# Performance work log

Hardware: AMD Instinct MI355X
Metric: run time of the kernel (lower is better)

The kernel has to match this reference:

```python
import jax, jax.numpy as jnp
import numpy as np

B, S, D = 2, 2048, 1024          # batch, seq, n_embd
E, GS, K = 8, 4, 2               # num_experts, group_size, top-k
H = 2 * D                        # hidden_dim of SharedExpertMLP
A = H // 16                      # adapt_dim = 128
G = E // GS                      # num_groups
LN_EPS = 1e-5


def _ln(z, g, b):
    mu = jnp.mean(z, -1, keepdims=True)
    v = jnp.mean((z - mu) ** 2, -1, keepdims=True)
    return (z - mu) * jax.lax.rsqrt(v + LN_EPS) * g + b


def setup_inputs() -> dict:
    key = jax.random.key(0)
    ks = jax.random.split(key, 12)
    s = float(D) ** -0.5
    sa = s * 0.01
    se = 0.01 * float(A) ** -0.5
    n = lambda k, shape, std: jax.random.normal(k, shape, jnp.float32) * std
    return {
        'x': jax.random.normal(ks[0], (B, S, D), jnp.float32),
        'W_up': n(ks[1], (H, D), s),
        'W_gate': n(ks[2], (H, D), s),
        'W_down': n(ks[3], (D, H), s),
        'W_pre': n(ks[4], (A, D), sa),
        'W_post': n(ks[5], (A, H), sa),
        'ln_g': jnp.ones((A,), jnp.float32),
        'ln_b': jnp.zeros((A,), jnp.float32),
        'W_aproj': n(ks[6], (H, A), sa),
        'A_exp': n(ks[7], (E, A, A), se),
        'ln_g_e': jnp.ones((E, A), jnp.float32),
        'ln_b_e': jnp.zeros((E, A), jnp.float32),
        'W_eproj': n(ks[8], (H, A), se),
        'W_oproj': n(ks[9], (D, H), se),
        'W_rg': n(ks[10], (G, D), 0.001),
        'W_re': n(ks[11], (GS, D), 0.001),
    }


def reference(x, W_up, W_gate, W_down, W_pre, W_post, ln_g, ln_b, W_aproj,
              A_exp, ln_g_e, ln_b_e, W_eproj, W_oproj, W_rg, W_re):
    silu = jax.nn.silu
    # ---- SharedExpertMLP ----
    up = x @ W_up.T
    gate = x @ W_gate.T
    hidden = silu(gate) * up                               # [B,S,H]
    adapt_in = _ln(x @ W_pre.T, ln_g, ln_b)                # [B,S,A]
    adapt_out = _ln(hidden @ W_post.T, ln_g, ln_b)         # [B,S,A]
    aw = silu(jnp.clip(jnp.einsum('bsa,bta->bst', adapt_in, adapt_out), -5.0, 5.0))
    adapt = jnp.einsum('bst,bta->bsa', aw, adapt_in)
    hidden = hidden + 0.1 * (adapt @ W_aproj.T)
    shared = hidden @ W_down.T                             # [B,S,D]
    # ---- HierarchicalRouter ----
    gl = x @ W_rg.T                                        # [B,S,G]
    gp = jax.nn.softmax(gl, -1)
    gw = jnp.max(gp, -1)                                   # top-1 group weight
    gidx = jnp.argmax(gp, -1)
    el = x @ W_re.T                                        # [B,S,GS]
    ep = jax.nn.softmax(el, -1)
    wloc, iloc = jax.lax.top_k(ep, K)
    eidx = gidx[..., None] * GS + iloc                     # [B,S,K] global expert ids
    wloc = wloc / (jnp.sum(wloc, -1, keepdims=True) + 1e-7)
    fw = gw[..., None] * wloc                              # final weights
    N = B * S
    dm = jnp.zeros((N, E), x.dtype).at[
        jnp.arange(N)[:, None], eidx.reshape(N, K)].set(fw.reshape(N, K))
    load = dm.sum(0)
    target = load.sum() / E
    router_loss = 0.001 * (jnp.mean((load - target) ** 2)
                           + jnp.mean(gl ** 2) + jnp.mean(el ** 2))
    dm = dm.reshape(B, S, E)
    # ---- ExpertGroup combine (vectorized masked gather/MLP/scatter) ----
    pre = x @ W_pre.T                                      # [B,S,A]
    h_e = jnp.einsum('bsa,eca->ebsc', pre, A_exp)          # per-expert adapter
    h_e = _ln(h_e, ln_g_e[:, None, None, :], ln_b_e[:, None, None, :])
    contrib = jnp.einsum('ebsc,hc->ebsh', h_e, W_eproj)    # [E,B,S,H]
    contrib = jnp.einsum('ebsh,dh->ebsd', contrib, W_oproj)
    w_e = jnp.moveaxis(dm, -1, 0)                          # [E,B,S]
    out = jnp.sum(dm, -1)[..., None] * shared + 0.1 * jnp.einsum('ebsd,ebs->bsd', contrib, w_e)
    return out, router_loss
```

## Files before the change

kernel.cpp:

```cpp
#include <hip/hip_runtime.h>
#include <hip/hip_bf16.h>
#include <math.h>

static constexpr int Bc = 2;
static constexpr int Sc = 2048;
static constexpr int Dc = 1024;
static constexpr int Hc = 2048;
static constexpr int Ac = 128;
static constexpr int Ec = 8;
static constexpr int GSc = 4;
static constexpr int Gc = 2;
static constexpr int Nc = Bc * Sc;
static constexpr float LN_EPSc = 1e-5f;
static constexpr int RBLK = 512;

typedef __attribute__((ext_vector_type(8))) short bf16x8;
typedef __attribute__((ext_vector_type(4))) float f32x4;
typedef __attribute__((ext_vector_type(4))) unsigned short us4;

__device__ __forceinline__ unsigned short f2b(float f) {
    union { float f; unsigned u; } v; v.f = f;
    return (unsigned short)((v.u + 0x7FFFu + ((v.u >> 16) & 1u)) >> 16);
}
__device__ __forceinline__ float b2f(unsigned short h) {
    union { unsigned u; float f; } v; v.u = (unsigned)h << 16; return v.f;
}
__device__ __forceinline__ float fsilu(float x) {
    return x / (1.f + __expf(-x));
}

#define GLOAD16(g, l) __builtin_amdgcn_global_load_lds( \
    (const __attribute__((address_space(1))) void*)(g), \
    (__attribute__((address_space(3))) void*)(l), 16, 0, 0)

template<int EPI>
__global__ __launch_bounds__(256, 4) void mgemm(
    const unsigned short* __restrict__ Ag, const unsigned short* __restrict__ Bg,
    void* __restrict__ Cg, int N, int K, int lda, int ldb, float alpha,
    float* __restrict__ aux, void* __restrict__ aux2,
    long long sA, long long sB, long long sC)
{
    __shared__ unsigned short As[128 * 64];
    __shared__ unsigned short Bs[128 * 64];
    const unsigned short* A = Ag + (long long)blockIdx.z * sA;
    const unsigned short* B = Bg + (long long)blockIdx.z * sB;
    float* fC = (float*)Cg + (long long)blockIdx.z * sC;
    unsigned short* usC = (unsigned short*)Cg + (long long)blockIdx.z * sC;

    const int nwg = gridDim.x * gridDim.y;
    const int flat = blockIdx.y * gridDim.x + blockIdx.x;
    const int swz = (flat & 7) * (nwg >> 3) + (flat >> 3);
    const int bx = swz % gridDim.x, by = swz / gridDim.x;
    const int bm = by * 128, bn = bx * 128;

    const int tid = threadIdx.x;
    const int w = tid >> 6, l = tid & 63;
    const int wm = (w >> 1) * 64, wn = (w & 1) * 64;
    const int fr = l & 15, g = l >> 4;

    const f32x4 zero = { 0.f, 0.f, 0.f, 0.f };
    f32x4 acc[4][4];
    #pragma unroll
    for (int i = 0; i < 4; ++i)
        #pragma unroll
        for (int j = 0; j < 4; ++j) acc[i][j] = zero;

    for (int k0 = 0; k0 < K; k0 += 64) {
        #pragma unroll
        for (int p = 0; p < 4; ++p) {
            const int c = p * 256 + tid;
            const int row = c >> 3;
            const int gch = (c & 7) ^ ((c >> 4) & 7);
            GLOAD16(A + (long long)(bm + row) * lda + k0 + gch * 8, &As[c * 8]);
            GLOAD16(B + (long long)(bn + row) * ldb + k0 + gch * 8, &Bs[c * 8]);
        }
        __syncthreads();
        #pragma unroll
        for (int h = 0; h < 2; ++h) {
            bf16x8 af[4], bfv[4];
            #pragma unroll
            for (int i = 0; i < 4; ++i) {
                const int ra = wm + i * 16 + fr;
                af[i]  = *(const bf16x8*)&As[ra * 64 + ((h * 4 + g) ^ ((ra >> 1) & 7)) * 8];
                const int rb = wn + i * 16 + fr;
                bfv[i] = *(const bf16x8*)&Bs[rb * 64 + ((h * 4 + g) ^ ((rb >> 1) & 7)) * 8];
            }
            #pragma unroll
            for (int i = 0; i < 4; ++i)
                #pragma unroll
                for (int j = 0; j < 4; ++j)
                    acc[i][j] = __builtin_amdgcn_mfma_f32_16x16x32_bf16(af[i], bfv[j], acc[i][j], 0, 0, 0);
        }
        __syncthreads();
    }

    if (EPI == 9) {
        if (bn < 2 * Hc) {
            #pragma unroll
            for (int mi = 0; mi < 4; ++mi) {
                #pragma unroll
                for (int j = 0; j < 2; ++j) {
                    #pragma unroll
                    for (int jr = 0; jr < 4; ++jr) {
                        const long long row = bm + wm + mi * 16 + g * 4 + jr;
                        const long long colh = ((bn + wn) >> 1) + j * 16 + fr;
                        const float gv = acc[mi][2 * j][jr];
                        const float uv = acc[mi][2 * j + 1][jr];
                        usC[row * Hc + colh] = f2b(fsilu(gv) * uv);
                    }
                }
            }
        } else {
            unsigned short* preb = (unsigned short*)aux2;
            #pragma unroll
            for (int mi = 0; mi < 4; ++mi) {
                #pragma unroll
                for (int ni = 0; ni < 4; ++ni) {
                    #pragma unroll
                    for (int jr = 0; jr < 4; ++jr) {
                        const long long row = bm + wm + mi * 16 + g * 4 + jr;
                        const int lc = wn + ni * 16 + fr;
                        const float v = acc[mi][ni][jr];
                        aux[row * Ac + lc] = v;
                        preb[row * Ac + lc] = f2b(v);
                    }
                }
            }
        }
    } else {
        #pragma unroll
        for (int mi = 0; mi < 4; ++mi)
            #pragma unroll
            for (int ni = 0; ni < 4; ++ni)
                #pragma unroll
                for (int jr = 0; jr < 4; ++jr) {
                    const long long row = bm + wm + mi * 16 + g * 4 + jr;
                    const long long col = bn + wn + ni * 16 + fr;
                    const long long idx = row * (long long)N + col;
                    const float v = acc[mi][ni][jr];
                    if (EPI == 0) fC[idx] = v;
                    else usC[idx] = f2b(alpha * v);
                }
    }
}

__global__ __launch_bounds__(256, 2) void mgemm64(
    const unsigned short* __restrict__ Ag, const unsigned short* __restrict__ Bg,
    float* __restrict__ Cg, int N, int K, int lda, int ldb, int zmod,
    long long sA1, long long sB1, long long sC1,
    long long sA2, long long sB2, long long sC2)
{
    __shared__ unsigned short As[128 * 32];
    __shared__ unsigned short Bs[64 * 32];
    const int z1 = blockIdx.z % zmod, z2 = blockIdx.z / zmod;
    const unsigned short* A = Ag + (long long)z1 * sA1 + (long long)z2 * sA2;
    const unsigned short* B = Bg + (long long)z1 * sB1 + (long long)z2 * sB2;
    float* fC = Cg + (long long)z1 * sC1 + (long long)z2 * sC2;

    const int nwg = gridDim.x * gridDim.y;
    const int flat = blockIdx.y * gridDim.x + blockIdx.x;
    const int swz = (flat & 7) * (nwg >> 3) + (flat >> 3);
    const int bx = swz % gridDim.x, by = swz / gridDim.x;
    const int bm = by * 128, bn = bx * 64;

    const int tid = threadIdx.x;
    const int w = tid >> 6, l = tid & 63;
    const int wm = (w >> 1) * 64, wn = (w & 1) * 32;
    const int fr = l & 15, g = l >> 4;

    const f32x4 zero = { 0.f, 0.f, 0.f, 0.f };
    f32x4 acc[4][2];
    #pragma unroll
    for (int i = 0; i < 4; ++i)
        #pragma unroll
        for (int j = 0; j < 2; ++j) acc[i][j] = zero;

    for (int k0 = 0; k0 < K; k0 += 32) {
        #pragma unroll
        for (int p = 0; p < 2; ++p) {
            const int c = p * 256 + tid;
            GLOAD16(A + (long long)(bm + (c >> 2)) * lda + k0 + (c & 3) * 8, &As[c * 8]);
        }
        GLOAD16(B + (long long)(bn + (tid >> 2)) * ldb + k0 + (tid & 3) * 8, &Bs[tid * 8]);
        __syncthreads();
        bf16x8 af[4], bfv[2];
        #pragma unroll
        for (int i = 0; i < 4; ++i)
            af[i]  = *(const bf16x8*)&As[(wm + i * 16 + fr) * 32 + g * 8];
        #pragma unroll
        for (int j = 0; j < 2; ++j)
            bfv[j] = *(const bf16x8*)&Bs[(wn + j * 16 + fr) * 32 + g * 8];
        #pragma unroll
        for (int i = 0; i < 4; ++i)
            #pragma unroll
            for (int j = 0; j < 2; ++j)
                acc[i][j] = __builtin_amdgcn_mfma_f32_16x16x32_bf16(af[i], bfv[j], acc[i][j], 0, 0, 0);
        __syncthreads();
    }

    #pragma unroll
    for (int mi = 0; mi < 4; ++mi)
        #pragma unroll
        for (int ni = 0; ni < 2; ++ni)
            #pragma unroll
            for (int jr = 0; jr < 4; ++jr) {
                const long long row = bm + wm + mi * 16 + g * 4 + jr;
                const long long col = bn + wn + ni * 16 + fr;
                fC[row * (long long)N + col] = acc[mi][ni][jr];
            }
}

__global__ __launch_bounds__(256, 2) void fadapt_k(
    const unsigned short* __restrict__ adapt_in,
    const unsigned short* __restrict__ adapt_out,
    const unsigned short* __restrict__ adapt_inT,
    float* __restrict__ partial)
{
    __shared__ unsigned short P_lds[4 * 64 * 32];

    const int b = blockIdx.z;
    const int q0 = blockIdx.y * 64;
    const int t0 = blockIdx.x * 256;

    const unsigned short* Qg = adapt_in + (long long)b * Sc * Ac;
    const unsigned short* Kg = adapt_out + (long long)b * Sc * Ac;
    const unsigned short* Vt = adapt_inT + (long long)b * Ac * Sc;

    const int tid = threadIdx.x;
    const int w = tid >> 6, l = tid & 63;
    const int wm = (w >> 1) * 32, wn = (w & 1) * 64;
    const int fr = l & 15, g = l >> 4;

    bf16x8 qf[2][4];
    #pragma unroll
    for (int i = 0; i < 2; ++i) {
        const long long ra = q0 + wm + i * 16 + fr;
        #pragma unroll
        for (int ks = 0; ks < 4; ++ks)
            qf[i][ks] = *(const bf16x8*)&Qg[ra * Ac + ks * 32 + g * 8];
    }

    const f32x4 zero = { 0.f, 0.f, 0.f, 0.f };
    f32x4 acc[2][4];
    #pragma unroll
    for (int i = 0; i < 2; ++i)
        #pragma unroll
        for (int j = 0; j < 4; ++j) acc[i][j] = zero;

    #pragma unroll 1
    for (int ts = 0; ts < 2; ++ts) {
        const int t1 = t0 + ts * 128;
        f32x4 sacc[2][4];
        #pragma unroll
        for (int i = 0; i < 2; ++i)
            #pragma unroll
            for (int j = 0; j < 4; ++j) sacc[i][j] = zero;
        #pragma unroll
        for (int ks = 0; ks < 4; ++ks) {
            bf16x8 bfv[4];
            #pragma unroll
            for (int j = 0; j < 4; ++j) {
                const long long rb = t1 + wn + j * 16 + fr;
                bfv[j] = *(const bf16x8*)&Kg[rb * Ac + ks * 32 + g * 8];
            }
            #pragma unroll
            for (int i = 0; i < 2; ++i)
                #pragma unroll
                for (int j = 0; j < 4; ++j)
                    sacc[i][j] = __builtin_amdgcn_mfma_f32_16x16x32_bf16(qf[i][ks], bfv[j], sacc[i][j], 0, 0, 0);
        }
        __syncthreads();
        #pragma unroll
        for (int mi = 0; mi < 2; ++mi) {
            #pragma unroll
            for (int ni = 0; ni < 4; ++ni) {
                const int t = wn + ni * 16 + fr;
                const int tl = t & 31;
                const int kbase = (t >> 5) * 2048;
                #pragma unroll
                for (int jr = 0; jr < 4; ++jr) {
                    const int row = wm + mi * 16 + g * 4 + jr;
                    float v = sacc[mi][ni][jr];
                    v = fminf(fmaxf(v, -5.f), 5.f);
                    const int pos = (((tl >> 3) ^ ((row >> 1) & 3)) << 3) + (tl & 7);
                    P_lds[kbase + row * 32 + pos] = f2b(fsilu(v));
                }
            }
        }
        __syncthreads();
        #pragma unroll
        for (int ks = 0; ks < 4; ++ks) {
            bf16x8 af[2], bfv[4];
            #pragma unroll
            for (int i = 0; i < 2; ++i) {
                const int ra = wm + i * 16 + fr;
                af[i] = *(const bf16x8*)&P_lds[ks * 2048 + ra * 32 + (g ^ ((ra >> 1) & 3)) * 8];
            }
            #pragma unroll
            for (int j = 0; j < 4; ++j) {
                const long long rb = wn + j * 16 + fr;
                bfv[j] = *(const bf16x8*)&Vt[rb * Sc + t1 + ks * 32 + g * 8];
            }
            #pragma unroll
            for (int i = 0; i < 2; ++i)
                #pragma unroll
                for (int j = 0; j < 4; ++j)
                    acc[i][j] = __builtin_amdgcn_mfma_f32_16x16x32_bf16(af[i], bfv[j], acc[i][j], 0, 0, 0);
        }
    }

    float* op = partial + ((long long)blockIdx.x * Bc + b) * Sc * Ac;
    #pragma unroll
    for (int mi = 0; mi < 2; ++mi)
        #pragma unroll
        for (int ni = 0; ni < 4; ++ni)
            #pragma unroll
            for (int jr = 0; jr < 4; ++jr) {
                const long long row = q0 + wm + mi * 16 + g * 4 + jr;
                const long long col = wn + ni * 16 + fr;
                op[row * Ac + col] = acc[mi][ni][jr];
            }
}

__global__ __launch_bounds__(256, 2) void final_k(
    const unsigned short* __restrict__ hidden, const unsigned short* __restrict__ Wd,
    const unsigned short* __restrict__ adaptb, const unsigned short* __restrict__ Wdap,
    const unsigned short* __restrict__ h2v, const unsigned short* __restrict__ Wopep,
    const float* __restrict__ dmsum, float* __restrict__ out)
{
    __shared__ unsigned short As[128 * 64];
    __shared__ unsigned short Bs[64 * 64];

    const int nwg = gridDim.x * gridDim.y;
    const int flat = blockIdx.y * gridDim.x + blockIdx.x;
    const int swz = (flat & 7) * (nwg >> 3) + (flat >> 3);
    const int bx = swz % gridDim.x, by = swz / gridDim.x;
    const int bm = by * 128, bn = bx * 64;

    const int tid = threadIdx.x;
    const int w = tid >> 6, l = tid & 63;
    const int wm = (w >> 1) * 64, wn = (w & 1) * 32;
    const int fr = l & 15, g = l >> 4;

    const f32x4 zero = { 0.f, 0.f, 0.f, 0.f };
    f32x4 acc[4][2];
    #pragma unroll
    for (int i = 0; i < 4; ++i)
        #pragma unroll
        for (int j = 0; j < 2; ++j) acc[i][j] = zero;

    const unsigned short* Ap[3] = { hidden, adaptb, h2v };
    const unsigned short* Bp[3] = { Wd, Wdap, Wopep };
    const int Ks[3] = { Hc, Ac, Ac };

    #pragma unroll 1
    for (int ph = 0; ph < 3; ++ph) {
        if (ph == 2) {
            #pragma unroll
            for (int mi = 0; mi < 4; ++mi)
                #pragma unroll
                for (int jr = 0; jr < 4; ++jr) {
                    const float rs = dmsum[bm + wm + mi * 16 + g * 4 + jr];
                    #pragma unroll
                    for (int ni = 0; ni < 2; ++ni) acc[mi][ni][jr] *= rs;
                }
        }
        const unsigned short* A = Ap[ph];
        const unsigned short* B = Bp[ph];
        const int K = Ks[ph];
        for (int k0 = 0; k0 < K; k0 += 64) {
            #pragma unroll
            for (int p = 0; p < 4; ++p) {
                const int c = p * 256 + tid;
                const int row = c >> 3;
                const int gch = (c & 7) ^ ((c >> 4) & 7);
                GLOAD16(A + (long long)(bm + row) * K + k0 + gch * 8, &As[c * 8]);
            }
            #pragma unroll
            for (int p = 0; p < 2; ++p) {
                const int c = p * 256 + tid;
                const int row = c >> 3;
                const int gch = (c & 7) ^ ((c >> 4) & 7);
                GLOAD16(B + (long long)(bn + row) * K + k0 + gch * 8, &Bs[c * 8]);
            }
            __syncthreads();
            #pragma unroll
            for (int h = 0; h < 2; ++h) {
                bf16x8 af[4], bfv[2];
                #pragma unroll
                for (int i = 0; i < 4; ++i) {
                    const int ra = wm + i * 16 + fr;
                    af[i]  = *(const bf16x8*)&As[ra * 64 + ((h * 4 + g) ^ ((ra >> 1) & 7)) * 8];
                }
                #pragma unroll
                for (int j = 0; j < 2; ++j) {
                    const int rb = wn + j * 16 + fr;
                    bfv[j] = *(const bf16x8*)&Bs[rb * 64 + ((h * 4 + g) ^ ((rb >> 1) & 7)) * 8];
                }
                #pragma unroll
                for (int i = 0; i < 4; ++i)
                    #pragma unroll
                    for (int j = 0; j < 2; ++j)
                        acc[i][j] = __builtin_amdgcn_mfma_f32_16x16x32_bf16(af[i], bfv[j], acc[i][j], 0, 0, 0);
            }
            __syncthreads();
        }
    }

    #pragma unroll
    for (int mi = 0; mi < 4; ++mi)
        #pragma unroll
        for (int ni = 0; ni < 2; ++ni)
            #pragma unroll
            for (int jr = 0; jr < 4; ++jr) {
                const long long row = bm + wm + mi * 16 + g * 4 + jr;
                const long long col = bn + wn + ni * 16 + fr;
                out[row * (long long)Dc + col] = acc[mi][ni][jr];
            }
}

template<int NP, int BF>
__global__ __launch_bounds__(256) void reduce_k(const float* __restrict__ in,
                                                void* __restrict__ outp,
                                                long long pstride, int n4, float alpha)
{
    for (int i = blockIdx.x * 256 + threadIdx.x; i < n4; i += gridDim.x * 256) {
        float4 s = ((const float4*)in)[i];
        #pragma unroll
        for (int p = 1; p < NP; ++p) {
            const float4 v = ((const float4*)(in + (long long)p * pstride))[i];
            s.x += v.x; s.y += v.y; s.z += v.z; s.w += v.w;
        }
        s.x *= alpha; s.y *= alpha; s.z *= alpha; s.w *= alpha;
        if (BF) {
            us4 o = { f2b(s.x), f2b(s.y), f2b(s.z), f2b(s.w) };
            ((us4*)outp)[i] = o;
        } else {
            ((float4*)outp)[i] = s;
        }
    }
}

struct PrepArgs {
    const float* csrc[4]; unsigned short* cdst[4]; int cn4[4];
    const float* Wg; const float* Wu; const float* Wpre; unsigned short* Wcat;
    const float* tin0; const float* tin1; unsigned short* tout0; unsigned short* tout1;
};
__global__ __launch_bounds__(256) void prep_k(PrepArgs a)
{
    __shared__ float T[64][68];
    const int y = blockIdx.y;
    if (y < 4) {
        const float4* s = (const float4*)a.csrc[y];
        us4* d = (us4*)a.cdst[y];
        const int n = a.cn4[y];
        for (int i = blockIdx.x * 256 + threadIdx.x; i < n; i += gridDim.x * 256) {
            const float4 v = s[i];
            us4 o;
            o.x = f2b(v.x); o.y = f2b(v.y); o.z = f2b(v.z); o.w = f2b(v.w);
            d[i] = o;
        }
    } else if (y == 4) {
        const int total = (2 * Hc + Ac) * 256;
        for (int u = blockIdx.x * 256 + threadIdx.x; u < total; u += gridDim.x * 256) {
            const int r = u >> 8, t = u & 255;
            const float* src; int srcrow;
            if (r < 2 * Hc) {
                const int b = r >> 5, wq = r & 31;
                src = (wq < 16) ? a.Wg : a.Wu;
                srcrow = b * 16 + (wq & 15);
            } else {
                src = a.Wpre;
                srcrow = r - 2 * Hc;
            }
            const float4 v = ((const float4*)(src + (long long)srcrow * Dc))[t];
            us4 o;
            o.x = f2b(v.x); o.y = f2b(v.y); o.z = f2b(v.z); o.w = f2b(v.w);
            ((us4*)(a.Wcat + (long long)r * Dc))[t] = o;
        }
    } else {
        const int rr = threadIdx.x >> 4, cc = (threadIdx.x & 15) * 4;
        for (int tb = blockIdx.x; tb < 128; tb += gridDim.x) {
            const int z = tb >> 6, rem = tb & 63;
            const int a0 = (rem >> 5) * 64, t0 = (rem & 31) * 64;
            const float* in = z ? a.tin1 : a.tin0;
            unsigned short* outp = z ? a.tout1 : a.tout0;
            __syncthreads();
            #pragma unroll
            for (int p = 0; p < 4; ++p) {
                const int row = p * 16 + rr;
                *(float4*)&T[row][cc] = *(const float4*)&in[(long long)(t0 + row) * Ac + a0 + cc];
            }
            __syncthreads();
            #pragma unroll
            for (int p = 0; p < 4; ++p) {
                const int ar = p * 16 + rr;
                us4 o;
                o.x = f2b(T[cc + 0][ar]); o.y = f2b(T[cc + 1][ar]);
                o.z = f2b(T[cc + 2][ar]); o.w = f2b(T[cc + 3][ar]);
                *(us4*)&outp[(long long)(a0 + ar) * Hc + t0 + cc] = o;
            }
        }
    }
}

__global__ __launch_bounds__(256) void lntr_k(const float* __restrict__ in,
                                              unsigned short* __restrict__ outn,
                                              unsigned short* __restrict__ outt,
                                              const float* __restrict__ gg,
                                              const float* __restrict__ bb)
{
    __shared__ unsigned short L[64][130];
    const int z = blockIdx.y;
    const int t0 = blockIdx.x * 64;
    const int wv = threadIdx.x >> 6, lane = threadIdx.x & 63;
    const float g0 = gg[lane], g1 = gg[lane + 64];
    const float b0 = bb[lane], b1 = bb[lane + 64];

    #pragma unroll 4
    for (int it = 0; it < 16; ++it) {
        const int row = wv * 16 + it;
        const long long gr = (long long)(z * Sc + t0 + row) * 128;
        const float z0 = in[gr + lane], z1 = in[gr + 64 + lane];
        float s = z0 + z1;
        #pragma unroll
        for (int o = 32; o > 0; o >>= 1) s += __shfl_xor(s, o, 64);
        const float mu = s * (1.f / 128.f);
        const float d0 = z0 - mu, d1 = z1 - mu;
        float v = d0 * d0 + d1 * d1;
        #pragma unroll
        for (int o = 32; o > 0; o >>= 1) v += __shfl_xor(v, o, 64);
        const float r = rsqrtf(v * (1.f / 128.f) + LN_EPSc);
        L[row][lane] = f2b(d0 * r * g0 + b0);
        L[row][lane + 64] = f2b(d1 * r * g1 + b1);
    }
    __syncthreads();
    {
        const int row = threadIdx.x >> 2, seg = (threadIdx.x & 3) * 32;
        #pragma unroll
        for (int j = 0; j < 8; ++j)
            *(us4*)&outn[(long long)(z * Sc + t0 + row) * 128 + seg + j * 4] =
                *(const us4*)&L[row][seg + j * 4];
    }
    {
        const int a = threadIdx.x >> 1, tt0 = (threadIdx.x & 1) * 32;
        #pragma unroll
        for (int j4 = 0; j4 < 8; ++j4) {
            us4 o;
            o.x = L[tt0 + j4 * 4 + 0][a]; o.y = L[tt0 + j4 * 4 + 1][a];
            o.z = L[tt0 + j4 * 4 + 2][a]; o.w = L[tt0 + j4 * 4 + 3][a];
            *(us4*)&outt[(long long)z * Ac * Sc + (long long)a * Sc + t0 + tt0 + j4 * 4] = o;
        }
    }
}

__global__ __launch_bounds__(64) void redln_k(const float* __restrict__ in,
                                              unsigned short* __restrict__ out,
                                              const float* __restrict__ gg,
                                              const float* __restrict__ bb,
                                              long long pstride)
{
    const int row = blockIdx.x;
    const int lane = threadIdx.x;
    float z0 = 0.f, z1 = 0.f;
    #pragma unroll
    for (int p = 0; p < 4; ++p) {
        z0 += in[p * pstride + (long long)row * 128 + lane];
        z1 += in[p * pstride + (long long)row * 128 + 64 + lane];
    }
    float s = z0 + z1;
    for (int o = 32; o > 0; o >>= 1) s += __shfl_xor(s, o, 64);
    const float mu = s * (1.f / 128.f);
    const float d0 = z0 - mu, d1 = z1 - mu;
    float v = d0 * d0 + d1 * d1;
    for (int o = 32; o > 0; o >>= 1) v += __shfl_xor(v, o, 64);
    const float r = rsqrtf(v * (1.f / 128.f) + LN_EPSc);
    out[(long long)row * 128 + lane] = f2b(d0 * r * gg[lane] + bb[lane]);
    out[(long long)row * 128 + 64 + lane] = f2b(d1 * r * gg[lane + 64] + bb[lane + 64]);
}

__global__ __launch_bounds__(256) void router_k(const float* __restrict__ x,
                                                const float* __restrict__ W_rg,
                                                const float* __restrict__ W_re,
                                                int* __restrict__ eidx, float* __restrict__ fw,
                                                float* __restrict__ dmsum,
                                                float* __restrict__ rpart,
                                                unsigned short* __restrict__ xb)
{
    const int wv = threadIdx.x >> 6;
    const int lane = threadIdx.x & 63;
    float load8[8] = {0.f, 0.f, 0.f, 0.f, 0.f, 0.f, 0.f, 0.f};
    float sqg = 0.f, sqe = 0.f;

    #pragma unroll
    for (int it = 0; it < 2; ++it) {
        const int t = blockIdx.x * 8 + wv * 2 + it;
        const float* xr = x + (long long)t * Dc;
        float a0 = 0, a1 = 0, a2 = 0, a3 = 0, a4 = 0, a5 = 0;
        #pragma unroll
        for (int j = 0; j < 16; ++j) {
            const int d = lane + 64 * j;
            const float xv = xr[d];
            xb[(long long)t * Dc + d] = f2b(xv);
            a0 += xv * W_rg[d];          a1 += xv * W_rg[Dc + d];
            a2 += xv * W_re[d];          a3 += xv * W_re[Dc + d];
            a4 += xv * W_re[2 * Dc + d]; a5 += xv * W_re[3 * Dc + d];
        }
        #pragma unroll
        for (int o = 32; o > 0; o >>= 1) {
            a0 += __shfl_xor(a0, o, 64); a1 += __shfl_xor(a1, o, 64);
            a2 += __shfl_xor(a2, o, 64); a3 += __shfl_xor(a3, o, 64);
            a4 += __shfl_xor(a4, o, 64); a5 += __shfl_xor(a5, o, 64);
        }
        if (lane == 0) {
            const float gl0 = a0, gl1 = a1;
            const float m = fmaxf(gl0, gl1);
            const float e0 = expf(gl0 - m), e1 = expf(gl1 - m);
            const float inv = 1.f / (e0 + e1);
            const float gp0 = e0 * inv, gp1 = e1 * inv;
            const int gidx = (gl1 > gl0) ? 1 : 0;
            const float gw = fmaxf(gp0, gp1);
            float el[4] = { a2, a3, a4, a5 };
            const float me = fmaxf(fmaxf(el[0], el[1]), fmaxf(el[2], el[3]));
            float ep[4]; float se = 0.f;
            #pragma unroll
            for (int i = 0; i < 4; ++i) { ep[i] = expf(el[i] - me); se += ep[i]; }
            const float invs = 1.f / se;
            #pragma unroll
            for (int i = 0; i < 4; ++i) ep[i] *= invs;
            int i0 = 0;
            #pragma unroll
            for (int i = 1; i < 4; ++i) if (ep[i] > ep[i0]) i0 = i;
            int i1 = -1;
            #pragma unroll
            for (int i = 0; i < 4; ++i) { if (i == i0) continue; if (i1 < 0 || ep[i] > ep[i1]) i1 = i; }
            const float w0 = ep[i0], w1 = ep[i1];
            const float sn = w0 + w1 + 1e-7f;
            const float f0 = gw * w0 / sn, f1 = gw * w1 / sn;
            const int ei0 = gidx * GSc + i0, ei1 = gidx * GSc + i1;
            eidx[t * 2] = ei0; eidx[t * 2 + 1] = ei1;
            fw[t * 2] = f0; fw[t * 2 + 1] = f1;
            dmsum[t] = f0 + f1;
            #pragma unroll
            for (int e = 0; e < 8; ++e)
                load8[e] += ((e == ei0) ? f0 : 0.f) + ((e == ei1) ? f1 : 0.f);
            sqg += gl0 * gl0 + gl1 * gl1;
            sqe += el[0] * el[0] + el[1] * el[1] + el[2] * el[2] + el[3] * el[3];
        }
    }
    __shared__ float sh[4][10];
    if (lane == 0) {
        #pragma unroll
        for (int e = 0; e < 8; ++e) sh[wv][e] = load8[e];
        sh[wv][8] = sqg; sh[wv][9] = sqe;
    }
    __syncthreads();
    if (threadIdx.x < 10) {
        rpart[blockIdx.x * 10 + threadIdx.x] =
            sh[0][threadIdx.x] + sh[1][threadIdx.x] + sh[2][threadIdx.x] + sh[3][threadIdx.x];
    }
}

__global__ __launch_bounds__(512) void loss_k(const float* __restrict__ rpart,
                                              float* __restrict__ out_loss)
{
    const int tid = threadIdx.x;
    const int lane = tid & 63, wv = tid >> 6;
    float v[10];
    #pragma unroll
    for (int c = 0; c < 10; ++c) v[c] = rpart[tid * 10 + c];
    #pragma unroll
    for (int o = 32; o > 0; o >>= 1)
        #pragma unroll
        for (int c = 0; c < 10; ++c) v[c] += __shfl_xor(v[c], o, 64);
    __shared__ float sh[8][10];
    if (lane == 0) {
        #pragma unroll
        for (int c = 0; c < 10; ++c) sh[wv][c] = v[c];
    }
    __syncthreads();
    if (tid == 0) {
        float load[8]; float sqg = 0.f, sqe = 0.f;
        #pragma unroll
        for (int e = 0; e < 8; ++e) load[e] = 0.f;
        for (int wvi = 0; wvi < 8; ++wvi) {
            #pragma unroll
            for (int e = 0; e < 8; ++e) load[e] += sh[wvi][e];
            sqg += sh[wvi][8]; sqe += sh[wvi][9];
        }
        float s = 0.f;
        for (int e = 0; e < Ec; ++e) s += load[e];
        const float tgt = s / (float)Ec;
        float var = 0.f;
        for (int e = 0; e < Ec; ++e) { const float d = load[e] - tgt; var += d * d; }
        var /= (float)Ec;
        const float l = var + sqg / (float)(Nc * Gc) + sqe / (float)(Nc * GSc);
        *out_loss = 0.001f * l;
    }
}

__global__ __launch_bounds__(128) void combine_k(const float* __restrict__ h_dense,
                                                 const float* __restrict__ ln_g_e,
                                                 const float* __restrict__ ln_b_e,
                                                 const int* __restrict__ eidx,
                                                 const float* __restrict__ fw,
                                                 unsigned short* __restrict__ h2)
{
    const int t = blockIdx.x;
    const int tid = threadIdx.x;
    __shared__ float red[2];

    float acc = 0.f;
    #pragma unroll
    for (int slot = 0; slot < 2; ++slot) {
        const int e = eidx[t * 2 + slot];
        const float w = fw[t * 2 + slot];
        const float h = h_dense[((long long)e * Nc + t) * 128 + tid];
        float v = h;
        for (int o = 32; o > 0; o >>= 1) v += __shfl_down(v, o, 64);
        if ((tid & 63) == 0) red[tid >> 6] = v;
        __syncthreads();
        const float mu = (red[0] + red[1]) * (1.f / 128.f);
        __syncthreads();
        const float d = h - mu;
        v = d * d;
        for (int o = 32; o > 0; o >>= 1) v += __shfl_down(v, o, 64);
        if ((tid & 63) == 0) red[tid >> 6] = v;
        __syncthreads();
        const float var = (red[0] + red[1]) * (1.f / 128.f);
        __syncthreads();
        acc += w * (d * rsqrtf(var + LN_EPSc) * ln_g_e[e * 128 + tid] + ln_b_e[e * 128 + tid]);
    }
    h2[(long long)t * 128 + tid] = f2b(acc);
}

extern "C" void kernel_launch(void* const* d_in, const int* in_sizes, int n_in,
                              void* d_out, int out_size, void* d_ws, size_t ws_size,
                              hipStream_t stream)
{
    const float* x       = (const float*)d_in[0];
    const float* W_up    = (const float*)d_in[1];
    const float* W_gate  = (const float*)d_in[2];
    const float* W_down  = (const float*)d_in[3];
    const float* W_pre   = (const float*)d_in[4];
    const float* W_post  = (const float*)d_in[5];
    const float* ln_g    = (const float*)d_in[6];
    const float* ln_b    = (const float*)d_in[7];
    const float* W_aproj = (const float*)d_in[8];
    const float* A_exp   = (const float*)d_in[9];
    const float* ln_g_e  = (const float*)d_in[10];
    const float* ln_b_e  = (const float*)d_in[11];
    const float* W_eproj = (const float*)d_in[12];
    const float* W_oproj = (const float*)d_in[13];
    const float* W_rg    = (const float*)d_in[14];
    const float* W_re    = (const float*)d_in[15];

    float* out = (float*)d_out;

    char* p = (char*)d_ws;
    auto alloc = [&](size_t bytes) { void* r = (void*)p; p += (bytes + 255) & ~(size_t)255; return r; };
    float* pre      = (float*)alloc((size_t)Nc * Ac * 4);
    float* h_dense  = (float*)alloc((size_t)Ec * Nc * Ac * 4);
    float* rpart    = (float*)alloc((size_t)RBLK * 10 * 4);
    float* fw       = (float*)alloc((size_t)Nc * 2 * 4);
    float* dmsum    = (float*)alloc((size_t)Nc * 4);
    int*   eidx     = (int*)alloc((size_t)Nc * 2 * 4);
    unsigned short* xb      = (unsigned short*)alloc((size_t)Nc * Dc * 2);
    unsigned short* Wcat_b  = (unsigned short*)alloc((size_t)(2 * Hc + Ac) * Dc * 2);
    unsigned short* Wd_b    = (unsigned short*)alloc((size_t)Dc * Hc * 2);
    unsigned short* Wop_b   = (unsigned short*)alloc((size_t)Dc * Hc * 2);
    unsigned short* Wpost_b = (unsigned short*)alloc((size_t)Ac * Hc * 2);
    unsigned short* WapT_b  = (unsigned short*)alloc((size_t)Ac * Hc * 2);
    unsigned short* WepT_b  = (unsigned short*)alloc((size_t)Ac * Hc * 2);
    unsigned short* Wdap_b  = (unsigned short*)alloc((size_t)Dc * Ac * 2);
    unsigned short* Wopep_b = (unsigned short*)alloc((size_t)Dc * Ac * 2);
    unsigned short* Aexp_b  = (unsigned short*)alloc((size_t)Ec * Ac * Ac * 2);
    unsigned short* pre_b   = (unsigned short*)alloc((size_t)Nc * Ac * 2);
    unsigned short* hidden  = (unsigned short*)alloc((size_t)Nc * Hc * 2);
    unsigned short* adapt_in  = (unsigned short*)alloc((size_t)Nc * Ac * 2);
    unsigned short* adapt_inT = (unsigned short*)alloc((size_t)Nc * Ac * 2);
    unsigned short* adapt_out = (unsigned short*)alloc((size_t)Nc * Ac * 2);
    unsigned short* adaptb    = (unsigned short*)alloc((size_t)Nc * Ac * 2);
    unsigned short* h2        = (unsigned short*)alloc((size_t)Nc * Ac * 2);

    float* wprepP = h_dense;
    float* postP  = h_dense;
    float* adaptP = h_dense;

    PrepArgs pa;
    pa.csrc[0] = W_down;  pa.cdst[0] = Wd_b;    pa.cn4[0] = Dc * Hc / 4;
    pa.csrc[1] = W_oproj; pa.cdst[1] = Wop_b;   pa.cn4[1] = Dc * Hc / 4;
    pa.csrc[2] = W_post;  pa.cdst[2] = Wpost_b; pa.cn4[2] = Ac * Hc / 4;
    pa.csrc[3] = A_exp;   pa.cdst[3] = Aexp_b;  pa.cn4[3] = Ec * Ac * Ac / 4;
    pa.Wg = W_gate; pa.Wu = W_up; pa.Wpre = W_pre; pa.Wcat = Wcat_b;
    pa.tin0 = W_aproj; pa.tin1 = W_eproj; pa.tout0 = WapT_b; pa.tout1 = WepT_b;
    prep_k<<<dim3(64, 6), 256, 0, stream>>>(pa);

    router_k<<<RBLK, 256, 0, stream>>>(x, W_rg, W_re, eidx, fw, dmsum, rpart, xb);
    loss_k<<<1, 512, 0, stream>>>(rpart, out + (size_t)Nc * Dc);

    mgemm64<<<dim3(2, 8, 8), 256, 0, stream>>>(Wd_b, WapT_b, wprepP, Ac, 512, Hc, Hc,
        2,
        (long long)Dc * Hc, (long long)Ac * Hc, (long long)Dc * Ac,
        512, 512, (long long)2 * Dc * Ac);
    reduce_k<4, 1><<<256, 256, 0, stream>>>(wprepP, Wdap_b,
        (long long)2 * Dc * Ac, 2 * Dc * Ac / 4, 0.1f);

    mgemm<9><<<dim3(33, 32), 256, 0, stream>>>(xb, Wcat_b, hidden, 2 * Hc + Ac, Dc, Dc, Dc, 0.f,
        pre, pre_b, 0, 0, 0);
    lntr_k<<<dim3(Sc / 64, Bc), 256, 0, stream>>>(pre, adapt_in, adapt_inT, ln_g, ln_b);

    mgemm64<<<dim3(2, 32, 4), 256, 0, stream>>>(hidden, Wpost_b, postP, Ac, 512, Hc, Hc,
        8, 512, 512, (long long)Nc * Ac, 0, 0, 0);
    redln_k<<<Nc, 64, 0, stream>>>(postP, adapt_out, ln_g, ln_b, (long long)Nc * Ac);

    mgemm64<<<dim3(2, 32, Ec), 256, 0, stream>>>(pre_b, Aexp_b, h_dense, Ac, Ac, Ac, Ac,
        16, 0, (long long)Ac * Ac, (long long)Nc * Ac, 0, 0, 0);
    combine_k<<<Nc, 128, 0, stream>>>(h_dense, ln_g_e, ln_b_e, eidx, fw, h2);

    fadapt_k<<<dim3(8, 32, 2), 256, 0, stream>>>(adapt_in, adapt_out, adapt_inT, adaptP);
    reduce_k<8, 1><<<512, 256, 0, stream>>>(adaptP, adaptb,
        (long long)2 * Sc * Ac, 2 * Sc * Ac / 4, 1.f);

    final_k<<<dim3(Dc / 64, Nc / 128), 256, 0, stream>>>(
        hidden, Wd_b, adaptb, Wdap_b, h2, Wopep_b, dmsum, out);
}
```

Before: 202.4 us.

## Double-buffer LDS tiles with async prefetch in GEMM and final kernels

Converts the K-loops of mgemm and final_k to a two-stage LDS ping-pong: the tile for step t+2 is issued with global_load_lds while step t is computed. Explicit vmcnt waits and raw s_barrier replace the per-step __syncthreads pair, so global-load latency overlaps with MFMA work. The doubled shared memory lowers the occupancy hints (mgemm 4→2 blocks, final_k 2→3). The risk is fewer resident waves, and the hand-counted vmcnt values only stay correct if the compiler issues no other vector memory ops inside the loop.

```diff
diff --git a/kernel.cpp b/kernel.cpp
--- a/kernel.cpp
+++ b/kernel.cpp
@@ -34,14 +34,14 @@
     (__attribute__((address_space(3))) void*)(l), 16, 0, 0)
 
 template<int EPI>
-__global__ __launch_bounds__(256, 4) void mgemm(
+__global__ __launch_bounds__(256, 2) void mgemm(
     const unsigned short* __restrict__ Ag, const unsigned short* __restrict__ Bg,
     void* __restrict__ Cg, int N, int K, int lda, int ldb, float alpha,
     float* __restrict__ aux, void* __restrict__ aux2,
     long long sA, long long sB, long long sC)
 {
-    __shared__ unsigned short As[128 * 64];
-    __shared__ unsigned short Bs[128 * 64];
+    __shared__ unsigned short As[2][128 * 64];
+    __shared__ unsigned short Bs[2][128 * 64];
     const unsigned short* A = Ag + (long long)blockIdx.z * sA;
     const unsigned short* B = Bg + (long long)blockIdx.z * sB;
     float* fC = (float*)Cg + (long long)blockIdx.z * sC;
@@ -65,25 +65,27 @@
         #pragma unroll
         for (int j = 0; j < 4; ++j) acc[i][j] = zero;
 
-    for (int k0 = 0; k0 < K; k0 += 64) {
+    auto stage = [&](int t, int buf) {
+        const int k0 = t << 6;
         #pragma unroll
         for (int p = 0; p < 4; ++p) {
             const int c = p * 256 + tid;
             const int row = c >> 3;
             const int gch = (c & 7) ^ ((c >> 4) & 7);
-            GLOAD16(A + (long long)(bm + row) * lda + k0 + gch * 8, &As[c * 8]);
-            GLOAD16(B + (long long)(bn + row) * ldb + k0 + gch * 8, &Bs[c * 8]);
-        }
-        __syncthreads();
+            GLOAD16(A + (long long)(bm + row) * lda + k0 + gch * 8, &As[buf][c * 8]);
+            GLOAD16(B + (long long)(bn + row) * ldb + k0 + gch * 8, &Bs[buf][c * 8]);
+        }
+    };
+    auto compute = [&](int cur) {
         #pragma unroll
         for (int h = 0; h < 2; ++h) {
             bf16x8 af[4], bfv[4];
             #pragma unroll
             for (int i = 0; i < 4; ++i) {
                 const int ra = wm + i * 16 + fr;
-                af[i]  = *(const bf16x8*)&As[ra * 64 + ((h * 4 + g) ^ ((ra >> 1) & 7)) * 8];
+                af[i]  = *(const bf16x8*)&As[cur][ra * 64 + ((h * 4 + g) ^ ((ra >> 1) & 7)) * 8];
                 const int rb = wn + i * 16 + fr;
-                bfv[i] = *(const bf16x8*)&Bs[rb * 64 + ((h * 4 + g) ^ ((rb >> 1) & 7)) * 8];
+                bfv[i] = *(const bf16x8*)&Bs[cur][rb * 64 + ((h * 4 + g) ^ ((rb >> 1) & 7)) * 8];
             }
             #pragma unroll
             for (int i = 0; i < 4; ++i)
@@ -91,8 +93,21 @@
                 for (int j = 0; j < 4; ++j)
                     acc[i][j] = __builtin_amdgcn_mfma_f32_16x16x32_bf16(af[i], bfv[j], acc[i][j], 0, 0, 0);
         }
-        __syncthreads();
-    }
+    };
+
+    const int nk = K >> 6;
+    stage(0, 0);
+    stage(1, 1);
+    for (int t = 0; t < nk - 1; ++t) {
+        asm volatile("s_waitcnt vmcnt(8)" ::: "memory");
+        __builtin_amdgcn_s_barrier();
+        compute(t & 1);
+        __builtin_amdgcn_s_barrier();
+        if (t + 2 < nk) stage(t + 2, t & 1);
+    }
+    asm volatile("s_waitcnt vmcnt(0)" ::: "memory");
+    __builtin_amdgcn_s_barrier();
+    compute((nk - 1) & 1);
 
     if (EPI == 9) {
         if (bn < 2 * Hc) {
@@ -322,14 +337,14 @@
             }
 }
 
-__global__ __launch_bounds__(256, 2) void final_k(
+__global__ __launch_bounds__(256, 3) void final_k(
     const unsigned short* __restrict__ hidden, const unsigned short* __restrict__ Wd,
     const unsigned short* __restrict__ adaptb, const unsigned short* __restrict__ Wdap,
     const unsigned short* __restrict__ h2v, const unsigned short* __restrict__ Wopep,
     const float* __restrict__ dmsum, float* __restrict__ out)
 {
-    __shared__ unsigned short As[128 * 64];
-    __shared__ unsigned short Bs[64 * 64];
+    __shared__ unsigned short As[2][128 * 64];
+    __shared__ unsigned short Bs[2][64 * 64];
 
     const int nwg = gridDim.x * gridDim.y;
     const int flat = blockIdx.y * gridDim.x + blockIdx.x;
@@ -368,34 +383,37 @@
         const unsigned short* A = Ap[ph];
         const unsigned short* B = Bp[ph];
         const int K = Ks[ph];
-        for (int k0 = 0; k0 < K; k0 += 64) {
+
+        auto stage = [&](int t, int buf) {
+            const int k0 = t << 6;
             #pragma unroll
             for (int p = 0; p < 4; ++p) {
                 const int c = p * 256 + tid;
                 const int row = c >> 3;
                 const int gch = (c & 7) ^ ((c >> 4) & 7);
-                GLOAD16(A + (long long)(bm + row) * K + k0 + gch * 8, &As[c * 8]);
+                GLOAD16(A + (long long)(bm + row) * K + k0 + gch * 8, &As[buf][c * 8]);
             }
             #pragma unroll
             for (int p = 0; p < 2; ++p) {
                 const int c = p * 256 + tid;
                 const int row = c >> 3;
                 const int gch = (c & 7) ^ ((c >> 4) & 7);
-                GLOAD16(B + (long long)(bn + row) * K + k0 + gch * 8, &Bs[c * 8]);
-            }
-            __syncthreads();
+                GLOAD16(B + (long long)(bn + row) * K + k0 + gch * 8, &Bs[buf][c * 8]);
+            }
+        };
+        auto compute = [&](int cur) {
             #pragma unroll
             for (int h = 0; h < 2; ++h) {
                 bf16x8 af[4], bfv[2];
                 #pragma unroll
                 for (int i = 0; i < 4; ++i) {
                     const int ra = wm + i * 16 + fr;
-                    af[i]  = *(const bf16x8*)&As[ra * 64 + ((h * 4 + g) ^ ((ra >> 1) & 7)) * 8];
+                    af[i]  = *(const bf16x8*)&As[cur][ra * 64 + ((h * 4 + g) ^ ((ra >> 1) & 7)) * 8];
                 }
                 #pragma unroll
                 for (int j = 0; j < 2; ++j) {
                     const int rb = wn + j * 16 + fr;
-                    bfv[j] = *(const bf16x8*)&Bs[rb * 64 + ((h * 4 + g) ^ ((rb >> 1) & 7)) * 8];
+                    bfv[j] = *(const bf16x8*)&Bs[cur][rb * 64 + ((h * 4 + g) ^ ((rb >> 1) & 7)) * 8];
                 }
                 #pragma unroll
                 for (int i = 0; i < 4; ++i)
@@ -403,8 +421,22 @@
                     for (int j = 0; j < 2; ++j)
                         acc[i][j] = __builtin_amdgcn_mfma_f32_16x16x32_bf16(af[i], bfv[j], acc[i][j], 0, 0, 0);
             }
-            __syncthreads();
-        }
+        };
+
+        const int nk = K >> 6;
+        stage(0, 0);
+        stage(1, 1);
+        for (int t = 0; t < nk - 1; ++t) {
+            asm volatile("s_waitcnt vmcnt(6)" ::: "memory");
+            __builtin_amdgcn_s_barrier();
+            compute(t & 1);
+            __builtin_amdgcn_s_barrier();
+            if (t + 2 < nk) stage(t + 2, t & 1);
+        }
+        asm volatile("s_waitcnt vmcnt(0)" ::: "memory");
+        __builtin_amdgcn_s_barrier();
+        compute((nk - 1) & 1);
+        __builtin_amdgcn_s_barrier();
     }
 
     #pragma unroll
```

After: 201.3 us. No clear change (-0.5%).
